# Performance work log

Hardware: AMD Instinct MI355X
Metric: run time of the kernel (lower is better)

Reference implementation:

```python
import jax, jax.numpy as jnp
import numpy as np

BIG = 1e8   # fill value used by to_dense_batch for missing neighbors in the original
EPS_W = 1e-8
EPS_BN = 1e-5


def setup_inputs() -> dict:
    key = jax.random.key(0)
    ks = jax.random.split(key, 8)
    N, S, Dc, Df = 16384, 4096, 256, 64
    fine_xyz = jax.random.normal(ks[0], (1, 3, N), dtype=jnp.float32)
    coarse_xyz = jax.random.normal(ks[1], (1, 3, S), dtype=jnp.float32)
    fine_piece_id = jnp.sort(jax.random.randint(ks[2], (1, 1, N), 0, 4))
    coarse_piece_id = jnp.sort(jax.random.randint(ks[3], (1, 1, S), 0, 4))
    fine_features = jax.random.normal(ks[4], (1, Df, N), dtype=jnp.float32)
    coarse_features = jax.random.normal(ks[5], (1, Dc, S), dtype=jnp.float32)
    # mlp stack: Conv1d(320->256), Conv1d(256->128), each with BatchNorm1d
    W1 = jax.random.normal(ks[6], (256, Dc + Df), dtype=jnp.float32) * 0.05
    b1 = jnp.zeros((256,), jnp.float32)
    g1 = jnp.ones((256,), jnp.float32)
    be1 = jnp.zeros((256,), jnp.float32)
    W2 = jax.random.normal(ks[7], (128, 256), dtype=jnp.float32) * 0.05
    b2 = jnp.zeros((128,), jnp.float32)
    g2 = jnp.ones((128,), jnp.float32)
    be2 = jnp.zeros((128,), jnp.float32)
    return dict(fine_xyz=fine_xyz, coarse_xyz=coarse_xyz,
                fine_piece_id=fine_piece_id, coarse_piece_id=coarse_piece_id,
                fine_features=fine_features, coarse_features=coarse_features,
                W1=W1, b1=b1, g1=g1, be1=be1, W2=W2, b2=b2, g2=g2, be2=be2)


def _bn_relu(x, gamma, beta):
    # x: [N, C]; BatchNorm1d in training mode -> batch stats over the N axis
    mu = jnp.mean(x, axis=0, keepdims=True)
    var = jnp.mean((x - mu) ** 2, axis=0, keepdims=True)  # biased var, as torch BN
    return jax.nn.relu((x - mu) * jax.lax.rsqrt(var + EPS_BN) * gamma + beta)


def reference(fine_xyz, coarse_xyz, fine_piece_id, coarse_piece_id,
              fine_features, coarse_features, W1, b1, g1, be1, W2, b2, g2, be2):
    fxyz = fine_xyz[0].T            # [N, 3]
    cxyz = coarse_xyz[0].T          # [S, 3]
    ff = fine_features[0].T         # [N, Df]
    cf = coarse_features[0].T       # [S, Dc]
    fid = fine_piece_id.reshape(-1)     # [N]
    cid = coarse_piece_id.reshape(-1)   # [S]

    # squared euclidean distances, masked to the same piece (knn with batch vectors)
    d2 = (jnp.sum(fxyz ** 2, -1)[:, None] + jnp.sum(cxyz ** 2, -1)[None, :]
          - 2.0 * fxyz @ cxyz.T)                       # [N, S]
    d2 = jnp.where(fid[:, None] != cid[None, :], BIG, d2)

    neg_d, idx = jax.lax.top_k(-d2, 3)                  # 3-NN per fine point
    dist = -neg_d                                       # [N, 3]

    w = 1.0 / (dist + EPS_W)
    w = w / jnp.sum(w, axis=1, keepdims=True)           # [N, 3]

    gathered = cf[idx]                                  # [N, 3, Dc]
    interp = jnp.sum(gathered * w[:, :, None], axis=1)  # [N, Dc]

    x = jnp.concatenate([interp, ff], axis=-1)          # [N, Dc+Df]
    x = _bn_relu(x @ W1.T + b1, g1, be1)                # [N, 256]
    x = _bn_relu(x @ W2.T + b2, g2, be2)                # [N, 128]
    return x.T[None]                                    # [1, 128, N]
```

## Files before the change

### kernel.cpp

```cpp
#include <hip/hip_runtime.h>
#include <hip/hip_bf16.h>

#define N_FINE   16384
#define S_COARSE 4096
#define DC       256
#define DF       64
#define K1       320
#define C1       256
#define C2       128
#define BIGF     1e8f
#define EPS_W    1e-8f
#define EPS_BN   1e-5f

typedef __attribute__((ext_vector_type(8))) short bf16x8;
typedef __attribute__((ext_vector_type(8))) unsigned short u16x8;
typedef __attribute__((ext_vector_type(4))) float f32x4;

#define OFF_RANGES 0
#define OFF_SUMS   256
#define OFF_SCALE1 3328
#define OFF_SHIFT1 4352
#define OFF_SCALE2 5376
#define OFF_SHIFT2 5888
#define OFF_CPACK  8192
#define OFF_CFT    73728
#define OFF_IDX3   4268032
#define OFF_W3     4464640
#define OFF_W1B    4661248
#define OFF_W2B    4825088
#define OFF_X      4890624
#define OFF_Y1     15376384
#define OFF_Y2     23764992

__device__ inline unsigned short f2bf_bits(float f) {
    __hip_bfloat16 h = __float2bfloat16(f);
    unsigned short u;
    __builtin_memcpy(&u, &h, 2);
    return u;
}

__global__ __launch_bounds__(256) void range_kernel(const int* __restrict__ cid,
                                                    int* __restrict__ ranges) {
    int t = threadIdx.x;
    if (t < 8) ranges[t] = 0;
    __syncthreads();
    for (int s = t; s < S_COARSE; s += 256) {
        int c = cid[s];
        if (s == 0 || cid[s - 1] != c) ranges[c] = s;
        if (s == S_COARSE - 1 || cid[s + 1] != c) ranges[4 + c] = s + 1;
    }
}

__global__ __launch_bounds__(256) void pack_coarse_kernel(const float* __restrict__ cxyz,
                                                          float4* __restrict__ cpack) {
    int s = blockIdx.x * 256 + threadIdx.x;
    float x = cxyz[s], y = cxyz[S_COARSE + s], z = cxyz[2 * S_COARSE + s];
    cpack[s] = make_float4(x, y, z, x * x + y * y + z * z);
}

__global__ __launch_bounds__(256) void transpose_cf_kernel(const float* __restrict__ cf,
                                                           float* __restrict__ cfT) {
    __shared__ float tile[32][33];
    int tx = threadIdx.x & 31, ty = threadIdx.x >> 5;
    int s0 = blockIdx.x * 32, c0 = blockIdx.y * 32;
    #pragma unroll
    for (int i = 0; i < 4; i++) {
        int c = c0 + ty + i * 8;
        tile[ty + i * 8][tx] = cf[c * S_COARSE + s0 + tx];
    }
    __syncthreads();
    #pragma unroll
    for (int i = 0; i < 4; i++) {
        int s = ty + i * 8;
        cfT[(s0 + s) * DC + c0 + tx] = tile[tx][s];
    }
}

__global__ __launch_bounds__(256) void cvtw_kernel(const float* __restrict__ W1,
                                                   const float* __restrict__ W2,
                                                   unsigned short* __restrict__ W1b,
                                                   unsigned short* __restrict__ W2b) {
    int i = blockIdx.x * 256 + threadIdx.x;
    if (i < C1 * K1) W1b[i] = f2bf_bits(W1[i]);
    if (i < C2 * C1) W2b[i] = f2bf_bits(W2[i]);
}

__global__ __launch_bounds__(256) void knn_kernel(const float* __restrict__ fxyz,
                                                  const int* __restrict__ fpid,
                                                  const float4* __restrict__ cpack,
                                                  const int* __restrict__ ranges,
                                                  int* __restrict__ idx3,
                                                  float* __restrict__ w3) {
    __shared__ float md[16][16][3];
    __shared__ int   mi[16][16][3];
    int t = threadIdx.x;
    int p = t & 15, ch = t >> 4;
    int n = blockIdx.x * 16 + p;
    int fid = fpid[n];
    float fx = fxyz[n], fy = fxyz[N_FINE + n], fz = fxyz[2 * N_FINE + n];
    float fn2 = fx * fx + fy * fy + fz * fz;
    int st = ranges[fid], en = ranges[4 + fid];
    int cnt = en - st;
    int L = (cnt + 15) >> 4;
    int cs = st + ch * L;
    int ce = min(cs + L, en);
    float d0 = BIGF, d1 = BIGF, d2v = BIGF;
    int i0 = -1, i1 = -1, i2 = -1;
    for (int s = cs; s < ce; ++s) {
        float4 c = cpack[s];
        float d = fn2 + c.w - 2.0f * (fx * c.x + fy * c.y + fz * c.z);
        if (d < d0)       { d2v = d1; i2 = i1; d1 = d0; i1 = i0; d0 = d; i0 = s; }
        else if (d < d1)  { d2v = d1; i2 = i1; d1 = d;  i1 = s; }
        else if (d < d2v) { d2v = d;  i2 = s; }
    }
    md[p][ch][0] = d0;  md[p][ch][1] = d1;  md[p][ch][2] = d2v;
    mi[p][ch][0] = i0;  mi[p][ch][1] = i1;  mi[p][ch][2] = i2;
    __syncthreads();
    if (t < 16) {
        d0 = d1 = d2v = BIGF; i0 = i1 = i2 = -1;
        for (int c = 0; c < 16; c++) {
            #pragma unroll
            for (int k = 0; k < 3; k++) {
                int ii = mi[t][c][k];
                if (ii < 0) continue;
                float d = md[t][c][k];
                if (d < d0)       { d2v = d1; i2 = i1; d1 = d0; i1 = i0; d0 = d; i0 = ii; }
                else if (d < d1)  { d2v = d1; i2 = i1; d1 = d;  i1 = ii; }
                else if (d < d2v) { d2v = d;  i2 = ii; }
            }
        }
        int cand = 0;
        while (i0 < 0 || i1 < 0 || i2 < 0) {
            if (cand >= st && cand < en) { cand = en; continue; }
            if (i0 < 0)      { i0 = cand; d0 = BIGF; }
            else if (i1 < 0) { i1 = cand; d1 = BIGF; }
            else             { i2 = cand; d2v = BIGF; }
            cand++;
        }
        float w0 = 1.0f / (d0 + EPS_W);
        float w1 = 1.0f / (d1 + EPS_W);
        float w2 = 1.0f / (d2v + EPS_W);
        float inv = 1.0f / (w0 + w1 + w2);
        idx3[n * 3 + 0] = i0; idx3[n * 3 + 1] = i1; idx3[n * 3 + 2] = i2;
        w3[n * 3 + 0] = w0 * inv; w3[n * 3 + 1] = w1 * inv; w3[n * 3 + 2] = w2 * inv;
    }
}

__global__ __launch_bounds__(256) void build_x_kernel(const int* __restrict__ idx3,
                                                      const float* __restrict__ w3,
                                                      const float* __restrict__ cfT,
                                                      const float* __restrict__ ff,
                                                      unsigned short* __restrict__ X) {
    int n = blockIdx.x, t = threadIdx.x;
    int i0 = idx3[n * 3], i1 = idx3[n * 3 + 1], i2 = idx3[n * 3 + 2];
    float w0 = w3[n * 3], w1 = w3[n * 3 + 1], w2 = w3[n * 3 + 2];
    float v = w0 * cfT[i0 * DC + t] + w1 * cfT[i1 * DC + t] + w2 * cfT[i2 * DC + t];
    X[n * K1 + t] = f2bf_bits(v);
    if (t < DF) X[n * K1 + DC + t] = f2bf_bits(ff[t * N_FINE + n]);
}

template <int KDIM, int NOUT, bool BN_IN, bool OUT_BF16>
__global__ __launch_bounds__(256) void mfma_gemm_kernel(
    const unsigned short* __restrict__ A,
    const unsigned short* __restrict__ B,
    const float* __restrict__ bias,
    const float* __restrict__ scale,
    const float* __restrict__ shift,
    void* __restrict__ Yout,
    float* __restrict__ sums, float* __restrict__ sumsq)
{
    __shared__ __align__(16) unsigned short As[4 * 128 * 8];
    __shared__ __align__(16) unsigned short Bs[4 * 64 * 8];
    int t = threadIdx.x;
    int m0 = blockIdx.x * 128, j0 = blockIdx.y * 64;
    int lane = t & 63, wid = t >> 6;
    int wm = (wid >> 1) * 64, wn = (wid & 1) * 32;

    int ksA = t & 3;
    int rowA0 = t >> 2;
    int rowA1 = 64 + rowA0;
    int fxw = ksA << 2;
    int gA0 = ksA * 128 + (rowA0 ^ fxw);
    int gA1 = ksA * 128 + (rowA1 ^ fxw);
    int gB  = ksA * 64 + (rowA0 ^ fxw);
    const unsigned short* pa0 = A + (size_t)(m0 + rowA0) * KDIM + ksA * 8;
    const unsigned short* pa1 = A + (size_t)(m0 + rowA1) * KDIM + ksA * 8;
    const unsigned short* pb  = B + (size_t)(j0 + rowA0) * KDIM + ksA * 8;

    f32x4 acc[4][2] = {};
    int ks = lane >> 4, r16 = lane & 15;
    int fxr = ks << 2;

    for (int kt = 0; kt < KDIM; kt += 32) {
        u16x8 va0 = *(const u16x8*)(pa0 + kt);
        u16x8 va1 = *(const u16x8*)(pa1 + kt);
        u16x8 vb  = *(const u16x8*)(pb + kt);
        if (BN_IN) {
            int kb = kt + ksA * 8;
            #pragma unroll
            for (int i = 0; i < 8; i++) {
                float sc = scale[kb + i], sh = shift[kb + i];
                float f0 = __uint_as_float(((unsigned)va0[i]) << 16);
                float f1 = __uint_as_float(((unsigned)va1[i]) << 16);
                va0[i] = f2bf_bits(fmaxf(fmaf(f0, sc, sh), 0.f));
                va1[i] = f2bf_bits(fmaxf(fmaf(f1, sc, sh), 0.f));
            }
        }
        __syncthreads();
        *(u16x8*)&As[gA0 * 8] = va0;
        *(u16x8*)&As[gA1 * 8] = va1;
        *(u16x8*)&Bs[gB * 8]  = vb;
        __syncthreads();
        bf16x8 af[4], bfr[2];
        #pragma unroll
        for (int mi = 0; mi < 4; mi++)
            af[mi] = *(const bf16x8*)&As[(ks * 128 + wm + mi * 16 + (r16 ^ fxr)) * 8];
        #pragma unroll
        for (int nj = 0; nj < 2; nj++)
            bfr[nj] = *(const bf16x8*)&Bs[(ks * 64 + wn + nj * 16 + (r16 ^ fxr)) * 8];
        #pragma unroll
        for (int mi = 0; mi < 4; mi++)
            #pragma unroll
            for (int nj = 0; nj < 2; nj++)
                acc[mi][nj] = __builtin_amdgcn_mfma_f32_16x16x32_bf16(af[mi], bfr[nj], acc[mi][nj], 0, 0, 0);
    }

    float sl[2] = {0.f, 0.f}, s2l[2] = {0.f, 0.f};
    #pragma unroll
    for (int nj = 0; nj < 2; nj++) {
        int n = j0 + wn + nj * 16 + r16;
        float bb = bias[n];
        #pragma unroll
        for (int mi = 0; mi < 4; mi++) {
            #pragma unroll
            for (int r = 0; r < 4; r++) {
                int m = m0 + wm + mi * 16 + ks * 4 + r;
                float o = acc[mi][nj][r] + bb;
                if (OUT_BF16) ((unsigned short*)Yout)[(size_t)m * NOUT + n] = f2bf_bits(o);
                else          ((float*)Yout)[(size_t)m * NOUT + n] = o;
                sl[nj] += o; s2l[nj] += o * o;
            }
        }
    }
    #pragma unroll
    for (int nj = 0; nj < 2; nj++) {
        sl[nj]  += __shfl_xor(sl[nj],  16, 64);
        sl[nj]  += __shfl_xor(sl[nj],  32, 64);
        s2l[nj] += __shfl_xor(s2l[nj], 16, 64);
        s2l[nj] += __shfl_xor(s2l[nj], 32, 64);
    }
    if (lane < 16) {
        atomicAdd(&sums[j0 + wn + lane],       sl[0]);
        atomicAdd(&sums[j0 + wn + 16 + lane],  sl[1]);
        atomicAdd(&sumsq[j0 + wn + lane],      s2l[0]);
        atomicAdd(&sumsq[j0 + wn + 16 + lane], s2l[1]);
    }
}

__global__ void finalize_kernel(const float* __restrict__ sums, const float* __restrict__ sumsq,
                                const float* __restrict__ g, const float* __restrict__ be,
                                float* __restrict__ scale, float* __restrict__ shift, int C) {
    int t = threadIdx.x;
    if (t < C) {
        float mean = sums[t] * (1.0f / N_FINE);
        float var = sumsq[t] * (1.0f / N_FINE) - mean * mean;
        float sc = g[t] * rsqrtf(var + EPS_BN);
        scale[t] = sc;
        shift[t] = be[t] - mean * sc;
    }
}

__global__ __launch_bounds__(256) void out_kernel(const float* __restrict__ Y2,
                                                  const float* __restrict__ scale2,
                                                  const float* __restrict__ shift2,
                                                  float* __restrict__ out) {
    __shared__ float tile[64][65];
    int t = threadIdx.x;
    int n0 = blockIdx.x * 64, c0 = blockIdx.y * 64;
    int cl = t & 63, rg = t >> 6;
    #pragma unroll
    for (int i = 0; i < 16; i++) {
        int r = rg + i * 4;
        tile[r][cl] = Y2[(n0 + r) * C2 + c0 + cl];
    }
    __syncthreads();
    #pragma unroll
    for (int i = 0; i < 16; i++) {
        int c = rg + i * 4;
        float v = fmaf(tile[cl][c], scale2[c0 + c], shift2[c0 + c]);
        out[(c0 + c) * N_FINE + n0 + cl] = fmaxf(v, 0.f);
    }
}

extern "C" void kernel_launch(void* const* d_in, const int* in_sizes, int n_in,
                              void* d_out, int out_size, void* d_ws, size_t ws_size,
                              hipStream_t stream) {
    const float* fine_xyz   = (const float*)d_in[0];
    const float* coarse_xyz = (const float*)d_in[1];
    const int*   fine_pid   = (const int*)d_in[2];
    const int*   coarse_pid = (const int*)d_in[3];
    const float* fine_feat  = (const float*)d_in[4];
    const float* coarse_feat= (const float*)d_in[5];
    const float* W1  = (const float*)d_in[6];
    const float* b1  = (const float*)d_in[7];
    const float* g1  = (const float*)d_in[8];
    const float* be1 = (const float*)d_in[9];
    const float* W2  = (const float*)d_in[10];
    const float* b2  = (const float*)d_in[11];
    const float* g2  = (const float*)d_in[12];
    const float* be2 = (const float*)d_in[13];
    float* out = (float*)d_out;

    char* ws = (char*)d_ws;
    int*    ranges = (int*)(ws + OFF_RANGES);
    float*  sums1  = (float*)(ws + OFF_SUMS);
    float*  sumsq1 = sums1 + 256;
    float*  sums2  = sums1 + 512;
    float*  sumsq2 = sums1 + 640;
    float*  scale1 = (float*)(ws + OFF_SCALE1);
    float*  shift1 = (float*)(ws + OFF_SHIFT1);
    float*  scale2 = (float*)(ws + OFF_SCALE2);
    float*  shift2 = (float*)(ws + OFF_SHIFT2);
    float4* cpack  = (float4*)(ws + OFF_CPACK);
    float*  cfT    = (float*)(ws + OFF_CFT);
    int*    idx3   = (int*)(ws + OFF_IDX3);
    float*  w3     = (float*)(ws + OFF_W3);
    unsigned short* W1b = (unsigned short*)(ws + OFF_W1B);
    unsigned short* W2b = (unsigned short*)(ws + OFF_W2B);
    unsigned short* X   = (unsigned short*)(ws + OFF_X);
    unsigned short* Y1  = (unsigned short*)(ws + OFF_Y1);
    float*          Y2  = (float*)(ws + OFF_Y2);

    hipMemsetAsync(ws + OFF_SUMS, 0, 768 * sizeof(float), stream);

    range_kernel<<<1, 256, 0, stream>>>(coarse_pid, ranges);
    pack_coarse_kernel<<<S_COARSE / 256, 256, 0, stream>>>(coarse_xyz, cpack);
    transpose_cf_kernel<<<dim3(S_COARSE / 32, DC / 32), 256, 0, stream>>>(coarse_feat, cfT);
    cvtw_kernel<<<(C1 * K1 + 255) / 256, 256, 0, stream>>>(W1, W2, W1b, W2b);
    knn_kernel<<<N_FINE / 16, 256, 0, stream>>>(fine_xyz, fine_pid, cpack, ranges, idx3, w3);
    build_x_kernel<<<N_FINE, 256, 0, stream>>>(idx3, w3, cfT, fine_feat, X);

    mfma_gemm_kernel<K1, C1, false, true><<<dim3(N_FINE / 128, C1 / 64), 256, 0, stream>>>(
        X, W1b, b1, nullptr, nullptr, Y1, sums1, sumsq1);
    finalize_kernel<<<1, 256, 0, stream>>>(sums1, sumsq1, g1, be1, scale1, shift1, C1);

    mfma_gemm_kernel<C1, C2, true, false><<<dim3(N_FINE / 128, C2 / 64), 256, 0, stream>>>(
        Y1, W2b, b2, scale1, shift1, Y2, sums2, sumsq2);
    finalize_kernel<<<1, 256, 0, stream>>>(sums2, sumsq2, g2, be2, scale2, shift2, C2);

    out_kernel<<<dim3(N_FINE / 64, C2 / 64), 256, 0, stream>>>(Y2, scale2, shift2, out);
}
```

Measured before the change: 191.1 us.

## Fuse interpolation gather into first GEMM and merge setup kernels

Removes the separate build_x kernel and the X buffer: the first GEMM now gathers the 3-NN coarse features, weights them, converts to bf16 and appends the fine features directly while staging its A tile, using a 32x256 tile per block. The four small setup kernels and the memset are merged into a single multi-role setup kernel to cut launch overhead. In exchange the GEMM tile shape changes (fewer rows per block, full output width), and the fine-feature loads inside it are strided and uncoalesced.

Measured after the change: 182.7 us. 4.4% less time.

```diff
diff --git a/kernel.cpp b/kernel.cpp
--- a/kernel.cpp
+++ b/kernel.cpp
@@ -28,9 +28,8 @@
 #define OFF_W3     4464640
 #define OFF_W1B    4661248
 #define OFF_W2B    4825088
-#define OFF_X      4890624
-#define OFF_Y1     15376384
-#define OFF_Y2     23764992
+#define OFF_Y1     4890624
+#define OFF_Y2     13279232
 
 __device__ inline unsigned short f2bf_bits(float f) {
     __hip_bfloat16 h = __float2bfloat16(f);
@@ -39,50 +38,46 @@
     return u;
 }
 
-__global__ __launch_bounds__(256) void range_kernel(const int* __restrict__ cid,
-                                                    int* __restrict__ ranges) {
-    int t = threadIdx.x;
-    if (t < 8) ranges[t] = 0;
-    __syncthreads();
-    for (int s = t; s < S_COARSE; s += 256) {
-        int c = cid[s];
-        if (s == 0 || cid[s - 1] != c) ranges[c] = s;
-        if (s == S_COARSE - 1 || cid[s + 1] != c) ranges[4 + c] = s + 1;
-    }
-}
-
-__global__ __launch_bounds__(256) void pack_coarse_kernel(const float* __restrict__ cxyz,
-                                                          float4* __restrict__ cpack) {
-    int s = blockIdx.x * 256 + threadIdx.x;
-    float x = cxyz[s], y = cxyz[S_COARSE + s], z = cxyz[2 * S_COARSE + s];
-    cpack[s] = make_float4(x, y, z, x * x + y * y + z * z);
-}
-
-__global__ __launch_bounds__(256) void transpose_cf_kernel(const float* __restrict__ cf,
-                                                           float* __restrict__ cfT) {
+__global__ __launch_bounds__(256) void setup_kernel(
+    const int* __restrict__ cid, int* __restrict__ ranges, float* __restrict__ sums,
+    const float* __restrict__ cxyz, float4* __restrict__ cpack,
+    const float* __restrict__ W1, const float* __restrict__ W2,
+    unsigned short* __restrict__ W1b, unsigned short* __restrict__ W2b,
+    const float* __restrict__ cf, float* __restrict__ cfT)
+{
     __shared__ float tile[32][33];
-    int tx = threadIdx.x & 31, ty = threadIdx.x >> 5;
-    int s0 = blockIdx.x * 32, c0 = blockIdx.y * 32;
-    #pragma unroll
-    for (int i = 0; i < 4; i++) {
-        int c = c0 + ty + i * 8;
-        tile[ty + i * 8][tx] = cf[c * S_COARSE + s0 + tx];
-    }
-    __syncthreads();
-    #pragma unroll
-    for (int i = 0; i < 4; i++) {
-        int s = ty + i * 8;
-        cfT[(s0 + s) * DC + c0 + tx] = tile[tx][s];
-    }
-}
-
-__global__ __launch_bounds__(256) void cvtw_kernel(const float* __restrict__ W1,
-                                                   const float* __restrict__ W2,
-                                                   unsigned short* __restrict__ W1b,
-                                                   unsigned short* __restrict__ W2b) {
-    int i = blockIdx.x * 256 + threadIdx.x;
-    if (i < C1 * K1) W1b[i] = f2bf_bits(W1[i]);
-    if (i < C2 * C1) W2b[i] = f2bf_bits(W2[i]);
+    int b = blockIdx.x, t = threadIdx.x;
+    if (b == 0) {
+        if (t < 8) ranges[t] = 0;
+        for (int i = t; i < 768; i += 256) sums[i] = 0.f;
+        __syncthreads();
+        for (int s = t; s < S_COARSE; s += 256) {
+            int c = cid[s];
+            if (s == 0 || cid[s - 1] != c) ranges[c] = s;
+            if (s == S_COARSE - 1 || cid[s + 1] != c) ranges[4 + c] = s + 1;
+        }
+    } else if (b <= 16) {
+        int s = (b - 1) * 256 + t;
+        float x = cxyz[s], y = cxyz[S_COARSE + s], z = cxyz[2 * S_COARSE + s];
+        cpack[s] = make_float4(x, y, z, x * x + y * y + z * z);
+    } else if (b <= 336) {
+        int i = (b - 17) * 256 + t;
+        W1b[i] = f2bf_bits(W1[i]);
+        if (i < C2 * C1) W2b[i] = f2bf_bits(W2[i]);
+    } else {
+        int lb = b - 337;
+        int tx = t & 31, ty = t >> 5;
+        int s0 = (lb & 127) * 32, c0 = (lb >> 7) * 32;
+        #pragma unroll
+        for (int i = 0; i < 4; i++)
+            tile[ty + i * 8][tx] = cf[(c0 + ty + i * 8) * S_COARSE + s0 + tx];
+        __syncthreads();
+        #pragma unroll
+        for (int i = 0; i < 4; i++) {
+            int s = ty + i * 8;
+            cfT[(s0 + s) * DC + c0 + tx] = tile[tx][s];
+        }
+    }
 }
 
 __global__ __launch_bounds__(256) void knn_kernel(const float* __restrict__ fxyz,
@@ -146,27 +141,129 @@
     }
 }
 
-__global__ __launch_bounds__(256) void build_x_kernel(const int* __restrict__ idx3,
-                                                      const float* __restrict__ w3,
-                                                      const float* __restrict__ cfT,
-                                                      const float* __restrict__ ff,
-                                                      unsigned short* __restrict__ X) {
-    int n = blockIdx.x, t = threadIdx.x;
-    int i0 = idx3[n * 3], i1 = idx3[n * 3 + 1], i2 = idx3[n * 3 + 2];
-    float w0 = w3[n * 3], w1 = w3[n * 3 + 1], w2 = w3[n * 3 + 2];
-    float v = w0 * cfT[i0 * DC + t] + w1 * cfT[i1 * DC + t] + w2 * cfT[i2 * DC + t];
-    X[n * K1 + t] = f2bf_bits(v);
-    if (t < DF) X[n * K1 + DC + t] = f2bf_bits(ff[t * N_FINE + n]);
-}
-
-template <int KDIM, int NOUT, bool BN_IN, bool OUT_BF16>
-__global__ __launch_bounds__(256) void mfma_gemm_kernel(
+__global__ __launch_bounds__(256) void gemm1_kernel(
+    const int* __restrict__ idx3, const float* __restrict__ w3,
+    const float* __restrict__ cfT, const float* __restrict__ ff,
+    const unsigned short* __restrict__ W1b, const float* __restrict__ bias,
+    unsigned short* __restrict__ Y1, float* __restrict__ sums, float* __restrict__ sumsq)
+{
+    __shared__ __align__(16) unsigned short As[4 * 32 * 8];
+    __shared__ __align__(16) unsigned short Bs[4 * 256 * 8];
+    __shared__ int   sI[32][3];
+    __shared__ float sWt[32][3];
+    int t = threadIdx.x;
+    int m0 = blockIdx.x * 32;
+    int lane = t & 63, wid = t >> 6;
+    int wn = wid * 64;
+
+    if (t < 32) {
+        sI[t][0]  = idx3[(m0 + t) * 3 + 0];
+        sI[t][1]  = idx3[(m0 + t) * 3 + 1];
+        sI[t][2]  = idx3[(m0 + t) * 3 + 2];
+        sWt[t][0] = w3[(m0 + t) * 3 + 0];
+        sWt[t][1] = w3[(m0 + t) * 3 + 1];
+        sWt[t][2] = w3[(m0 + t) * 3 + 2];
+    }
+    int ksA = t & 3, rowA = t >> 2;
+    int fxw = ksA << 2;
+    int gA = ksA * 32 + (rowA ^ fxw);
+    int rowB = t;
+    f32x4 acc[2][4] = {};
+    int ks = lane >> 4, r16 = lane & 15, fxr = ks << 2;
+    __syncthreads();
+
+    for (int kt = 0; kt < K1; kt += 32) {
+        u16x8 va;
+        if (t < 128) {
+            int k0 = kt + ksA * 8;
+            if (k0 < DC) {
+                int i0 = sI[rowA][0], i1 = sI[rowA][1], i2 = sI[rowA][2];
+                float w0 = sWt[rowA][0], w1 = sWt[rowA][1], w2 = sWt[rowA][2];
+                const float* c0p = &cfT[i0 * DC + k0];
+                const float* c1p = &cfT[i1 * DC + k0];
+                const float* c2p = &cfT[i2 * DC + k0];
+                float4 a0 = *(const float4*)c0p, a1 = *(const float4*)(c0p + 4);
+                float4 b0 = *(const float4*)c1p, b1 = *(const float4*)(c1p + 4);
+                float4 e0 = *(const float4*)c2p, e1 = *(const float4*)(c2p + 4);
+                va[0] = f2bf_bits(w0 * a0.x + w1 * b0.x + w2 * e0.x);
+                va[1] = f2bf_bits(w0 * a0.y + w1 * b0.y + w2 * e0.y);
+                va[2] = f2bf_bits(w0 * a0.z + w1 * b0.z + w2 * e0.z);
+                va[3] = f2bf_bits(w0 * a0.w + w1 * b0.w + w2 * e0.w);
+                va[4] = f2bf_bits(w0 * a1.x + w1 * b1.x + w2 * e1.x);
+                va[5] = f2bf_bits(w0 * a1.y + w1 * b1.y + w2 * e1.y);
+                va[6] = f2bf_bits(w0 * a1.z + w1 * b1.z + w2 * e1.z);
+                va[7] = f2bf_bits(w0 * a1.w + w1 * b1.w + w2 * e1.w);
+            } else {
+                int c = k0 - DC;
+                #pragma unroll
+                for (int i = 0; i < 8; i++)
+                    va[i] = f2bf_bits(ff[(c + i) * N_FINE + m0 + rowA]);
+            }
+        }
+        u16x8 vb[4];
+        #pragma unroll
+        for (int kb = 0; kb < 4; kb++)
+            vb[kb] = *(const u16x8*)&W1b[(size_t)rowB * K1 + kt + kb * 8];
+        __syncthreads();
+        if (t < 128) *(u16x8*)&As[gA * 8] = va;
+        #pragma unroll
+        for (int kb = 0; kb < 4; kb++)
+            *(u16x8*)&Bs[(kb * 256 + (rowB ^ (kb << 2))) * 8] = vb[kb];
+        __syncthreads();
+        bf16x8 af[2], bfr[4];
+        #pragma unroll
+        for (int mi = 0; mi < 2; mi++)
+            af[mi] = *(const bf16x8*)&As[(ks * 32 + ((mi * 16 + r16) ^ fxr)) * 8];
+        #pragma unroll
+        for (int nj = 0; nj < 4; nj++)
+            bfr[nj] = *(const bf16x8*)&Bs[(ks * 256 + ((wn + nj * 16 + r16) ^ fxr)) * 8];
+        #pragma unroll
+        for (int mi = 0; mi < 2; mi++)
+            #pragma unroll
+            for (int nj = 0; nj < 4; nj++)
+                acc[mi][nj] = __builtin_amdgcn_mfma_f32_16x16x32_bf16(af[mi], bfr[nj], acc[mi][nj], 0, 0, 0);
+    }
+
+    float sl[4] = {0.f, 0.f, 0.f, 0.f}, s2l[4] = {0.f, 0.f, 0.f, 0.f};
+    #pragma unroll
+    for (int nj = 0; nj < 4; nj++) {
+        int n = wn + nj * 16 + r16;
+        float bb = bias[n];
+        #pragma unroll
+        for (int mi = 0; mi < 2; mi++) {
+            #pragma unroll
+            for (int r = 0; r < 4; r++) {
+                int m = m0 + mi * 16 + ks * 4 + r;
+                float o = acc[mi][nj][r] + bb;
+                Y1[(size_t)m * C1 + n] = f2bf_bits(o);
+                sl[nj] += o; s2l[nj] += o * o;
+            }
+        }
+    }
+    #pragma unroll
+    for (int nj = 0; nj < 4; nj++) {
+        sl[nj]  += __shfl_xor(sl[nj],  16, 64);
+        sl[nj]  += __shfl_xor(sl[nj],  32, 64);
+        s2l[nj] += __shfl_xor(s2l[nj], 16, 64);
+        s2l[nj] += __shfl_xor(s2l[nj], 32, 64);
+    }
+    if (lane < 16) {
+        #pragma unroll
+        for (int nj = 0; nj < 4; nj++) {
+            atomicAdd(&sums[wn + nj * 16 + lane],  sl[nj]);
+            atomicAdd(&sumsq[wn + nj * 16 + lane], s2l[nj]);
+        }
+    }
+}
+
+template <int KDIM, int NOUT>
+__global__ __launch_bounds__(256) void mfma_gemm2_kernel(
     const unsigned short* __restrict__ A,
     const unsigned short* __restrict__ B,
     const float* __restrict__ bias,
     const float* __restrict__ scale,
     const float* __restrict__ shift,
-    void* __restrict__ Yout,
+    float* __restrict__ Yout,
     float* __restrict__ sums, float* __restrict__ sumsq)
 {
     __shared__ __align__(16) unsigned short As[4 * 128 * 8];
@@ -195,16 +292,14 @@
         u16x8 va0 = *(const u16x8*)(pa0 + kt);
         u16x8 va1 = *(const u16x8*)(pa1 + kt);
         u16x8 vb  = *(const u16x8*)(pb + kt);
-        if (BN_IN) {
-            int kb = kt + ksA * 8;
-            #pragma unroll
-            for (int i = 0; i < 8; i++) {
-                float sc = scale[kb + i], sh = shift[kb + i];
-                float f0 = __uint_as_float(((unsigned)va0[i]) << 16);
-                float f1 = __uint_as_float(((unsigned)va1[i]) << 16);
-                va0[i] = f2bf_bits(fmaxf(fmaf(f0, sc, sh), 0.f));
-                va1[i] = f2bf_bits(fmaxf(fmaf(f1, sc, sh), 0.f));
-            }
+        int kb = kt + ksA * 8;
+        #pragma unroll
+        for (int i = 0; i < 8; i++) {
+            float sc = scale[kb + i], sh = shift[kb + i];
+            float f0 = __uint_as_float(((unsigned)va0[i]) << 16);
+            float f1 = __uint_as_float(((unsigned)va1[i]) << 16);
+            va0[i] = f2bf_bits(fmaxf(fmaf(f0, sc, sh), 0.f));
+            va1[i] = f2bf_bits(fmaxf(fmaf(f1, sc, sh), 0.f));
         }
         __syncthreads();
         *(u16x8*)&As[gA0 * 8] = va0;
@@ -236,8 +331,7 @@
             for (int r = 0; r < 4; r++) {
                 int m = m0 + wm + mi * 16 + ks * 4 + r;
                 float o = acc[mi][nj][r] + bb;
-                if (OUT_BF16) ((unsigned short*)Yout)[(size_t)m * NOUT + n] = f2bf_bits(o);
-                else          ((float*)Yout)[(size_t)m * NOUT + n] = o;
+                Yout[(size_t)m * NOUT + n] = o;
                 sl[nj] += o; s2l[nj] += o * o;
             }
         }
@@ -327,24 +421,19 @@
     float*  w3     = (float*)(ws + OFF_W3);
     unsigned short* W1b = (unsigned short*)(ws + OFF_W1B);
     unsigned short* W2b = (unsigned short*)(ws + OFF_W2B);
-    unsigned short* X   = (unsigned short*)(ws + OFF_X);
     unsigned short* Y1  = (unsigned short*)(ws + OFF_Y1);
     float*          Y2  = (float*)(ws + OFF_Y2);
 
-    hipMemsetAsync(ws + OFF_SUMS, 0, 768 * sizeof(float), stream);
-
-    range_kernel<<<1, 256, 0, stream>>>(coarse_pid, ranges);
-    pack_coarse_kernel<<<S_COARSE / 256, 256, 0, stream>>>(coarse_xyz, cpack);
-    transpose_cf_kernel<<<dim3(S_COARSE / 32, DC / 32), 256, 0, stream>>>(coarse_feat, cfT);
-    cvtw_kernel<<<(C1 * K1 + 255) / 256, 256, 0, stream>>>(W1, W2, W1b, W2b);
+    setup_kernel<<<1361, 256, 0, stream>>>(coarse_pid, ranges, sums1,
+                                           coarse_xyz, cpack, W1, W2, W1b, W2b,
+                                           coarse_feat, cfT);
     knn_kernel<<<N_FINE / 16, 256, 0, stream>>>(fine_xyz, fine_pid, cpack, ranges, idx3, w3);
-    build_x_kernel<<<N_FINE, 256, 0, stream>>>(idx3, w3, cfT, fine_feat, X);
-
-    mfma_gemm_kernel<K1, C1, false, true><<<dim3(N_FINE / 128, C1 / 64), 256, 0, stream>>>(
-        X, W1b, b1, nullptr, nullptr, Y1, sums1, sumsq1);
+
+    gemm1_kernel<<<N_FINE / 32, 256, 0, stream>>>(idx3, w3, cfT, fine_feat,
+                                                  W1b, b1, Y1, sums1, sumsq1);
     finalize_kernel<<<1, 256, 0, stream>>>(sums1, sumsq1, g1, be1, scale1, shift1, C1);
 
-    mfma_gemm_kernel<C1, C2, true, false><<<dim3(N_FINE / 128, C2 / 64), 256, 0, stream>>>(
+    mfma_gemm2_kernel<C1, C2><<<dim3(N_FINE / 128, C2 / 64), 256, 0, stream>>>(
         Y1, W2b, b2, scale1, shift1, Y2, sums2, sumsq2);
     finalize_kernel<<<1, 256, 0, stream>>>(sums2, sumsq2, g2, be2, scale2, shift2, C2);
 
```
